# Kernel tuning notes

Measured on AMD Instinct MI355X. Metric: run time of the kernel, lower is better.

## Reference

```python
import jax, jax.numpy as jnp
import numpy as np

S = 14
L_COORD = 5.0
L_NOOBJ = 0.5


def setup_inputs() -> dict:
    key = jax.random.key(0)
    k1, k2, k3 = jax.random.split(key, 3)
    B = 4096
    pred = jax.random.uniform(k1, (B, S, S, 30), dtype=jnp.float32)
    target = jax.random.uniform(k2, (B, S, S, 30), dtype=jnp.float32)
    # matching real YOLO targets where most cells are background.
    gate = jax.random.uniform(k3, (B, S, S))
    conf = jnp.where(gate > 0.85, target[..., 4], 0.0)
    target = target.at[..., 4].set(conf)
    return {"pred_tensor": pred, "target_tensor": target}


def _to_xyxy(b):
    # b: (..., 5) [x, y, w, h, c] -> (..., 4) [x1, y1, x2, y2]
    c = b[..., :2] / 14.0
    half = 0.5 * b[..., 2:4]
    return jnp.concatenate([c - half, c + half], axis=-1)


def _iou_2v1(pbox, tbox):
    # pbox: (B,S,S,2,4) xyxy, tbox: (B,S,S,4) -> iou (B,S,S,2)
    lt = jnp.maximum(pbox[..., :2], tbox[..., None, :2])
    rb = jnp.minimum(pbox[..., 2:], tbox[..., None, 2:])
    wh = jnp.clip(rb - lt, 0.0)
    inter = wh[..., 0] * wh[..., 1]
    a1 = (pbox[..., 2] - pbox[..., 0]) * (pbox[..., 3] - pbox[..., 1])
    a2 = (tbox[..., 2] - tbox[..., 0]) * (tbox[..., 3] - tbox[..., 1])
    return inter / (a1 + a2[..., None] - inter)


def reference(pred_tensor, target_tensor):
    pred, target = pred_tensor, target_tensor
    N = pred.shape[0]
    dt = pred.dtype
    coo = (target[..., 4] > 0).astype(dt)          # (B,S,S) object cells
    noo = 1.0 - coo                                # background cells

    # no-object confidence loss over both conf slots (indices 4 and 9)
    noobj_loss = jnp.sum(noo * ((pred[..., 4] - target[..., 4]) ** 2
                                + (pred[..., 9] - target[..., 9]) ** 2))

    # boxes: (B,S,S,2,5)
    pb = pred[..., :10].reshape(pred.shape[0], S, S, 2, 5)
    tb = target[..., :10].reshape(target.shape[0], S, S, 2, 5)

    # IoU of both predicted boxes vs first target box; detached (torch uses .data)
    iou = jax.lax.stop_gradient(_iou_2v1(_to_xyxy(pb), _to_xyxy(tb[..., 0, :])))
    resp = jax.nn.one_hot(jnp.argmax(iou, axis=-1), 2, dtype=dt)  # (B,S,S,2)
    max_iou = jnp.max(iou, axis=-1)                               # (B,S,S)

    p_resp = jnp.einsum('bijk,bijkc->bijc', resp, pb)  # responsible pred box
    t_resp = jnp.einsum('bijk,bijkc->bijc', resp, tb)  # matching target box
    conf_not_resp = jnp.einsum('bijk,bijk->bij', 1.0 - resp, pb[..., 4])

    contain_loss = jnp.sum(coo * (p_resp[..., 4] - max_iou) ** 2)
    not_contain_loss = jnp.sum(coo * conf_not_resp ** 2)  # target conf forced to 0

    loc_loss = jnp.sum(coo[..., None] * ((p_resp[..., :2] - t_resp[..., :2]) ** 2
               + (jnp.sqrt(p_resp[..., 2:4]) - jnp.sqrt(t_resp[..., 2:4])) ** 2))

    class_loss = jnp.sum(coo[..., None] * (pred[..., 10:] - target[..., 10:]) ** 2)

    total = (L_COORD * loc_loss + contain_loss
             + L_NOOBJ * (noobj_loss + not_contain_loss) + class_loss) / N
    return total
```

## Files before the change

kernel.cpp:

```cpp
#include <hip/hip_runtime.h>


#ifndef NBLOCKS
#define NBLOCKS 1024
#endif

__global__ __launch_bounds__(256) void yolo_cells(
    const float* __restrict__ pred, const float* __restrict__ targ,
    float* __restrict__ partial, int ncells)
{
    float acc = 0.0f;
    for (int idx = blockIdx.x * blockDim.x + threadIdx.x; idx < ncells;
         idx += gridDim.x * blockDim.x) {
        const float2* p2 = reinterpret_cast<const float2*>(pred) + (size_t)idx * 15;
        const float2* t2 = reinterpret_cast<const float2*>(targ) + (size_t)idx * 15;
        float p[30], t[30];
#pragma unroll
        for (int i = 0; i < 15; ++i) {
            float2 v = p2[i]; p[2*i] = v.x; p[2*i+1] = v.y;
            float2 u = t2[i]; t[2*i] = u.x; t[2*i+1] = u.y;
        }

        const bool coo = t[4] > 0.0f;
        float cell;
        if (!coo) {
            float d4 = p[4] - t[4];
            float d9 = p[9] - t[9];
            cell = 0.5f * (d4 * d4 + d9 * d9);
        } else {
            const float inv14 = 1.0f / 14.0f;
            float p0x1 = p[0]*inv14 - 0.5f*p[2], p0y1 = p[1]*inv14 - 0.5f*p[3];
            float p0x2 = p[0]*inv14 + 0.5f*p[2], p0y2 = p[1]*inv14 + 0.5f*p[3];
            float p1x1 = p[5]*inv14 - 0.5f*p[7], p1y1 = p[6]*inv14 - 0.5f*p[8];
            float p1x2 = p[5]*inv14 + 0.5f*p[7], p1y2 = p[6]*inv14 + 0.5f*p[8];
            float tx1  = t[0]*inv14 - 0.5f*t[2], ty1  = t[1]*inv14 - 0.5f*t[3];
            float tx2  = t[0]*inv14 + 0.5f*t[2], ty2  = t[1]*inv14 + 0.5f*t[3];

            float at = (tx2 - tx1) * (ty2 - ty1);

            float w0 = fmaxf(fminf(p0x2, tx2) - fmaxf(p0x1, tx1), 0.0f);
            float h0 = fmaxf(fminf(p0y2, ty2) - fmaxf(p0y1, ty1), 0.0f);
            float inter0 = w0 * h0;
            float a0 = (p0x2 - p0x1) * (p0y2 - p0y1);
            float iou0 = inter0 / (a0 + at - inter0);

            float w1 = fmaxf(fminf(p1x2, tx2) - fmaxf(p1x1, tx1), 0.0f);
            float h1 = fmaxf(fminf(p1y2, ty2) - fmaxf(p1y1, ty1), 0.0f);
            float inter1 = w1 * h1;
            float a1 = (p1x2 - p1x1) * (p1y2 - p1y1);
            float iou1 = inter1 / (a1 + at - inter1);

            bool  r1      = iou1 > iou0;
            float max_iou = fmaxf(iou0, iou1);

            float prx = r1 ? p[5] : p[0], pry = r1 ? p[6] : p[1];
            float prw = r1 ? p[7] : p[2], prh = r1 ? p[8] : p[3];
            float prc = r1 ? p[9] : p[4];
            float trx = r1 ? t[5] : t[0], try_ = r1 ? t[6] : t[1];
            float trw = r1 ? t[7] : t[2], trh = r1 ? t[8] : t[3];
            float cnr = r1 ? p[4] : p[9];

            float dc = prc - max_iou;
            float contain = dc * dc;
            float not_contain = cnr * cnr;

            float dx = prx - trx, dy = pry - try_;
            float dw = sqrtf(prw) - sqrtf(trw);
            float dh = sqrtf(prh) - sqrtf(trh);
            float loc = dx * dx + dy * dy + dw * dw + dh * dh;

            float cls = 0.0f;
#pragma unroll
            for (int k = 10; k < 30; ++k) {
                float d = p[k] - t[k];
                cls += d * d;
            }
            cell = 5.0f * loc + contain + 0.5f * not_contain + cls;
        }
        acc += cell;
    }

    __shared__ float sm[256];
    sm[threadIdx.x] = acc;
    __syncthreads();
#pragma unroll
    for (int s = 128; s > 0; s >>= 1) {
        if (threadIdx.x < s) sm[threadIdx.x] += sm[threadIdx.x + s];
        __syncthreads();
    }
    if (threadIdx.x == 0) partial[blockIdx.x] = sm[0];
}

__global__ __launch_bounds__(256) void yolo_final(
    const float* __restrict__ partial, int n, float* __restrict__ out, float invN)
{
    __shared__ float sm[256];
    float acc = 0.0f;
    for (int i = threadIdx.x; i < n; i += 256) acc += partial[i];
    sm[threadIdx.x] = acc;
    __syncthreads();
#pragma unroll
    for (int s = 128; s > 0; s >>= 1) {
        if (threadIdx.x < s) sm[threadIdx.x] += sm[threadIdx.x + s];
        __syncthreads();
    }
    if (threadIdx.x == 0) out[0] = sm[0] * invN;
}

extern "C" void kernel_launch(void* const* d_in, const int* in_sizes, int n_in,
                              void* d_out, int out_size, void* d_ws, size_t ws_size,
                              hipStream_t stream) {
    const float* pred = (const float*)d_in[0];
    const float* targ = (const float*)d_in[1];
    float* out = (float*)d_out;
    float* partial = (float*)d_ws;

    const int ncells = in_sizes[0] / 30;
    const int B      = ncells / 196;
    const float invN = 1.0f / (float)B;

    yolo_cells<<<NBLOCKS, 256, 0, stream>>>(pred, targ, partial, ncells);
    yolo_final<<<1, 256, 0, stream>>>(partial, NBLOCKS, out, invN);
}
```

Before: 42.56 us.

## Process two cells per thread with float4 loads and one-shot grid

Each thread now handles a pair of adjacent cells, loading 60 floats per tensor with 16-byte float4 loads instead of 8-byte float2 loads. The grid-stride loop is replaced by one pair per thread, with a grid sized to cover all pairs (about 1568 blocks) and a matching final reduction. All loads are issued before any compute, separated by a compiler barrier, to raise memory-level parallelism. Register pressure rises from 60 to 120 live loaded floats, which may lower occupancy. An odd cell count would leave the last cell unprocessed.

```diff
diff --git a/kernel.cpp b/kernel.cpp
--- a/kernel.cpp
+++ b/kernel.cpp
@@ -1,83 +1,89 @@
 #include <hip/hip_runtime.h>
 
 
-#ifndef NBLOCKS
-#define NBLOCKS 1024
-#endif
+__device__ __forceinline__ float cell_loss(const float* __restrict__ p,
+                                           const float* __restrict__ t)
+{
+    const bool coo = t[4] > 0.0f;
+    if (!coo) {
+        float d4 = p[4] - t[4];
+        float d9 = p[9] - t[9];
+        return 0.5f * (d4 * d4 + d9 * d9);
+    }
+    const float inv14 = 1.0f / 14.0f;
+    float p0x1 = p[0]*inv14 - 0.5f*p[2], p0y1 = p[1]*inv14 - 0.5f*p[3];
+    float p0x2 = p[0]*inv14 + 0.5f*p[2], p0y2 = p[1]*inv14 + 0.5f*p[3];
+    float p1x1 = p[5]*inv14 - 0.5f*p[7], p1y1 = p[6]*inv14 - 0.5f*p[8];
+    float p1x2 = p[5]*inv14 + 0.5f*p[7], p1y2 = p[6]*inv14 + 0.5f*p[8];
+    float tx1  = t[0]*inv14 - 0.5f*t[2], ty1  = t[1]*inv14 - 0.5f*t[3];
+    float tx2  = t[0]*inv14 + 0.5f*t[2], ty2  = t[1]*inv14 + 0.5f*t[3];
+
+    float at = (tx2 - tx1) * (ty2 - ty1);
+
+    float w0 = fmaxf(fminf(p0x2, tx2) - fmaxf(p0x1, tx1), 0.0f);
+    float h0 = fmaxf(fminf(p0y2, ty2) - fmaxf(p0y1, ty1), 0.0f);
+    float inter0 = w0 * h0;
+    float a0 = (p0x2 - p0x1) * (p0y2 - p0y1);
+    float iou0 = inter0 / (a0 + at - inter0);
+
+    float w1 = fmaxf(fminf(p1x2, tx2) - fmaxf(p1x1, tx1), 0.0f);
+    float h1 = fmaxf(fminf(p1y2, ty2) - fmaxf(p1y1, ty1), 0.0f);
+    float inter1 = w1 * h1;
+    float a1 = (p1x2 - p1x1) * (p1y2 - p1y1);
+    float iou1 = inter1 / (a1 + at - inter1);
+
+    bool  r1      = iou1 > iou0;
+    float max_iou = fmaxf(iou0, iou1);
+
+    float prx = r1 ? p[5] : p[0], pry = r1 ? p[6] : p[1];
+    float prw = r1 ? p[7] : p[2], prh = r1 ? p[8] : p[3];
+    float prc = r1 ? p[9] : p[4];
+    float trx = r1 ? t[5] : t[0], try_ = r1 ? t[6] : t[1];
+    float trw = r1 ? t[7] : t[2], trh = r1 ? t[8] : t[3];
+    float cnr = r1 ? p[4] : p[9];
+
+    float dc = prc - max_iou;
+    float contain = dc * dc;
+    float not_contain = cnr * cnr;
+
+    float dx = prx - trx, dy = pry - try_;
+    float dw = sqrtf(prw) - sqrtf(trw);
+    float dh = sqrtf(prh) - sqrtf(trh);
+    float loc = dx * dx + dy * dy + dw * dw + dh * dh;
+
+    float cls = 0.0f;
+#pragma unroll
+    for (int k = 10; k < 30; ++k) {
+        float d = p[k] - t[k];
+        cls += d * d;
+    }
+    return 5.0f * loc + contain + 0.5f * not_contain + cls;
+}
 
 __global__ __launch_bounds__(256) void yolo_cells(
     const float* __restrict__ pred, const float* __restrict__ targ,
-    float* __restrict__ partial, int ncells)
+    float* __restrict__ partial, int npairs)
 {
     float acc = 0.0f;
-    for (int idx = blockIdx.x * blockDim.x + threadIdx.x; idx < ncells;
-         idx += gridDim.x * blockDim.x) {
-        const float2* p2 = reinterpret_cast<const float2*>(pred) + (size_t)idx * 15;
-        const float2* t2 = reinterpret_cast<const float2*>(targ) + (size_t)idx * 15;
-        float p[30], t[30];
+    const int pair = blockIdx.x * 256 + threadIdx.x;
+    if (pair < npairs) {
+        float p[60], t[60];
+        const float4* P4 = reinterpret_cast<const float4*>(pred) + (size_t)pair * 15;
+        const float4* T4 = reinterpret_cast<const float4*>(targ) + (size_t)pair * 15;
 #pragma unroll
         for (int i = 0; i < 15; ++i) {
-            float2 v = p2[i]; p[2*i] = v.x; p[2*i+1] = v.y;
-            float2 u = t2[i]; t[2*i] = u.x; t[2*i+1] = u.y;
+            float4 v = P4[i];
+            p[4*i+0] = v.x; p[4*i+1] = v.y; p[4*i+2] = v.z; p[4*i+3] = v.w;
         }
+#pragma unroll
+        for (int i = 0; i < 15; ++i) {
+            float4 v = T4[i];
+            t[4*i+0] = v.x; t[4*i+1] = v.y; t[4*i+2] = v.z; t[4*i+3] = v.w;
+        }
+        asm volatile("" ::: "memory");
 
-        const bool coo = t[4] > 0.0f;
-        float cell;
-        if (!coo) {
-            float d4 = p[4] - t[4];
-            float d9 = p[9] - t[9];
-            cell = 0.5f * (d4 * d4 + d9 * d9);
-        } else {
-            const float inv14 = 1.0f / 14.0f;
-            float p0x1 = p[0]*inv14 - 0.5f*p[2], p0y1 = p[1]*inv14 - 0.5f*p[3];
-            float p0x2 = p[0]*inv14 + 0.5f*p[2], p0y2 = p[1]*inv14 + 0.5f*p[3];
-            float p1x1 = p[5]*inv14 - 0.5f*p[7], p1y1 = p[6]*inv14 - 0.5f*p[8];
-            float p1x2 = p[5]*inv14 + 0.5f*p[7], p1y2 = p[6]*inv14 + 0.5f*p[8];
-            float tx1  = t[0]*inv14 - 0.5f*t[2], ty1  = t[1]*inv14 - 0.5f*t[3];
-            float tx2  = t[0]*inv14 + 0.5f*t[2], ty2  = t[1]*inv14 + 0.5f*t[3];
-
-            float at = (tx2 - tx1) * (ty2 - ty1);
-
-            float w0 = fmaxf(fminf(p0x2, tx2) - fmaxf(p0x1, tx1), 0.0f);
-            float h0 = fmaxf(fminf(p0y2, ty2) - fmaxf(p0y1, ty1), 0.0f);
-            float inter0 = w0 * h0;
-            float a0 = (p0x2 - p0x1) * (p0y2 - p0y1);
-            float iou0 = inter0 / (a0 + at - inter0);
-
-            float w1 = fmaxf(fminf(p1x2, tx2) - fmaxf(p1x1, tx1), 0.0f);
-            float h1 = fmaxf(fminf(p1y2, ty2) - fmaxf(p1y1, ty1), 0.0f);
-            float inter1 = w1 * h1;
-            float a1 = (p1x2 - p1x1) * (p1y2 - p1y1);
-            float iou1 = inter1 / (a1 + at - inter1);
-
-            bool  r1      = iou1 > iou0;
-            float max_iou = fmaxf(iou0, iou1);
-
-            float prx = r1 ? p[5] : p[0], pry = r1 ? p[6] : p[1];
-            float prw = r1 ? p[7] : p[2], prh = r1 ? p[8] : p[3];
-            float prc = r1 ? p[9] : p[4];
-            float trx = r1 ? t[5] : t[0], try_ = r1 ? t[6] : t[1];
-            float trw = r1 ? t[7] : t[2], trh = r1 ? t[8] : t[3];
-            float cnr = r1 ? p[4] : p[9];
-
-            float dc = prc - max_iou;
-            float contain = dc * dc;
-            float not_contain = cnr * cnr;
-
-            float dx = prx - trx, dy = pry - try_;
-            float dw = sqrtf(prw) - sqrtf(trw);
-            float dh = sqrtf(prh) - sqrtf(trh);
-            float loc = dx * dx + dy * dy + dw * dw + dh * dh;
-
-            float cls = 0.0f;
-#pragma unroll
-            for (int k = 10; k < 30; ++k) {
-                float d = p[k] - t[k];
-                cls += d * d;
-            }
-            cell = 5.0f * loc + contain + 0.5f * not_contain + cls;
-        }
-        acc += cell;
+        acc  = cell_loss(p,      t);
+        acc += cell_loss(p + 30, t + 30);
     }
 
     __shared__ float sm[256];
@@ -119,6 +125,9 @@
     const int B      = ncells / 196;
     const float invN = 1.0f / (float)B;
 
-    yolo_cells<<<NBLOCKS, 256, 0, stream>>>(pred, targ, partial, ncells);
-    yolo_final<<<1, 256, 0, stream>>>(partial, NBLOCKS, out, invN);
+    const int npairs = ncells / 2;
+    const int nblocks = (npairs + 255) / 256;
+
+    yolo_cells<<<nblocks, 256, 0, stream>>>(pred, targ, partial, npairs);
+    yolo_final<<<1, 256, 0, stream>>>(partial, nblocks, out, invN);
 }
```

After: 38.10 us. 1.12x faster.
